# Kernel optimization log

Hardware: AMD Instinct MI355X
Metric: run time of the kernel (lower is better)

## Reference

```python
import jax, jax.numpy as jnp
import numpy as np

K = 3          # attention window (kernel_size)
PAD = 1        # padding
C_IN = 256
C_OUT = 512    # final_channel
N_SPECIES, N_FAMILY, N_ORDER = 64500, 510, 100


def setup_inputs() -> dict:
    key = jax.random.key(0)
    ks = jax.random.split(key, 16)
    B, H, W = 4, 64, 64
    std = 0.01  # per torch.nn.init.normal_(std=0.01)
    inp = {
        "x": jax.random.normal(ks[0], (B, C_IN, H, W), jnp.float32),
        "wq": jax.random.normal(ks[1], (C_OUT, C_IN), jnp.float32) * std,
        "bq": jnp.zeros((C_OUT,), jnp.float32),
        "wk": jax.random.normal(ks[2], (C_OUT, C_IN), jnp.float32) * std,
        "bk": jnp.zeros((C_OUT,), jnp.float32),
        "wv": jax.random.normal(ks[3], (C_OUT, C_IN), jnp.float32) * std,
        "bv": jnp.zeros((C_OUT,), jnp.float32),
        "rel_h": jax.random.normal(ks[4], (C_OUT // 2, K), jnp.float32),
        "rel_w": jax.random.normal(ks[5], (C_OUT // 2, K), jnp.float32),
        "w_species": jax.random.normal(ks[6], (N_SPECIES, C_OUT), jnp.float32) * std,
        "b_species": jnp.zeros((N_SPECIES,), jnp.float32),
        "w_family": jax.random.normal(ks[7], (N_FAMILY, C_OUT), jnp.float32) * std,
        "b_family": jnp.zeros((N_FAMILY,), jnp.float32),
        "w_order": jax.random.normal(ks[8], (N_ORDER, C_OUT), jnp.float32) * std,
        "b_order": jnp.zeros((N_ORDER,), jnp.float32),
    }
    return inp


def _patches(t, H, W):
    # t: padded [B, C, H+2, W+2] -> [B, C, H, W, K, K] (unfold order: kh then kw)
    return jnp.stack([
        jnp.stack([t[:, :, i:i + H, j:j + W] for j in range(K)], axis=-1)
        for i in range(K)], axis=-2)


def _attention_conv(x, wq, bq, wk, bk, wv, bv, rel_h, rel_w):
    B, _, H, W = x.shape
    q = jnp.einsum('oc,bchw->bohw', wq, x) + bq[None, :, None, None]
    k = jnp.einsum('oc,bchw->bohw', wk, x) + bk[None, :, None, None]
    v = jnp.einsum('oc,bchw->bohw', wv, x) + bv[None, :, None, None]
    pad = ((0, 0), (0, 0), (PAD, PAD), (PAD, PAD))
    kp = _patches(jnp.pad(k, pad), H, W)                       # [B,C,H,W,K,K]
    vp = _patches(jnp.pad(v, pad), H, W).reshape(B, C_OUT, H, W, K * K)
    half = C_OUT // 2
    kp = jnp.concatenate([
        kp[:, :half] + rel_h[None, :, None, None, :, None],    # rel over kh
        kp[:, half:] + rel_w[None, :, None, None, None, :],    # rel over kw
    ], axis=1).reshape(B, C_OUT, H, W, K * K)
    attn = jax.nn.softmax(q[..., None] * kp, axis=-1)          # per-channel softmax over window
    return jnp.einsum('bchwk,bchwk->bchw', attn, vp)


def reference(x, wq, bq, wk, bk, wv, bv, rel_h, rel_w,
              w_species, b_species, w_family, b_family, w_order, b_order):
    att = jax.nn.relu(_attention_conv(x, wq, bq, wk, bk, wv, bv, rel_h, rel_w))
    pooled = att.mean(axis=(2, 3))                             # AdaptiveAvgPool2d((1,1)) -> [B, 512]
    sp = pooled @ w_species.T + b_species
    fa = pooled @ w_family.T + b_family
    od = pooled @ w_order.T + b_order
    # concatenated per-level logits (species | family | order)
    return jnp.concatenate([sp, fa, od], axis=1)
```

## Files before the change

### kernel.cpp

```cpp
#include <hip/hip_runtime.h>
#include <stdint.h>

#define HW    4096
#define CIN   256
#define COUT  512
#define NSPE  64500
#define NFAM  510
#define NORD  100
#define NOUT  65110

typedef __attribute__((ext_vector_type(8))) short bf16x8;
typedef __attribute__((ext_vector_type(4))) float f32x4;
typedef __attribute__((address_space(3))) uint32_t lds_u32;
typedef __attribute__((address_space(1))) const uint32_t glob_u32;

__device__ __forceinline__ short f32_to_bf16(float f) {
    uint32_t u = __float_as_uint(f);
    u += 0x7fffu + ((u >> 16) & 1u);
    return (short)(u >> 16);
}
__device__ __forceinline__ float lo16(uint32_t u) {
    return __uint_as_float(u << 16);
}
__device__ __forceinline__ float hi16(uint32_t u) {
    return __uint_as_float(u & 0xffff0000u);
}


__global__ __launch_bounds__(256) void convert_kernel(
    const float* __restrict__ x,
    const float* __restrict__ wq, const float* __restrict__ wk,
    const float* __restrict__ wv,
    short* __restrict__ Xt, short* __restrict__ Wt)
{
    const int t = threadIdx.x;
    __shared__ float lds[32][128];

    if (blockIdx.z < 4) {
        const int kt = blockIdx.x, nt = blockIdx.y, b = blockIdx.z;
        #pragma unroll
        for (int j = 0; j < 16; ++j) {
            int idx = j * 256 + t;
            int c = idx >> 7, p = idx & 127;
            lds[c][p] = x[((size_t)b * CIN + kt * 32 + c) * HW + nt * 128 + p];
        }
        __syncthreads();

        const int n = t >> 1;
        short* out = Xt + (((size_t)(b * 32 + nt) * 8 + kt) << 12);
        union { short s[16]; int4 v[2]; } pk;
        #pragma unroll
        for (int j = 0; j < 16; ++j) {
            int e  = t * 16 + j;
            int sp = (e >> 3) & 3;
            int i  = e & 7;
            int k  = ((sp ^ ((n >> 1) & 3)) << 3) + i;
            pk.s[j] = f32_to_bf16(lds[k][n]);
        }
        int4* dst = (int4*)(out + t * 16);
        dst[0] = pk.v[0];
        dst[1] = pk.v[1];
    } else {
        if (blockIdx.y >= 12) return;
        const int kt = blockIdx.x, mt = blockIdx.y & 3, mat = blockIdx.y >> 2;
        const float* __restrict__ W = (mat == 0) ? wq : (mat == 1) ? wk : wv;
        const int m = t >> 1;
        short* out = Wt + (((size_t)(mat * 4 + mt) * 8 + kt) << 12);

        union { short s[16]; int4 v[2]; } pk;
        #pragma unroll
        for (int j = 0; j < 16; ++j) {
            int e  = t * 16 + j;
            int sp = (e >> 3) & 3;
            int i  = e & 7;
            int k  = ((sp ^ ((m >> 1) & 3)) << 3) + i;
            pk.s[j] = f32_to_bf16(W[(size_t)(mt * 128 + m) * CIN + kt * 32 + k]);
        }
        int4* dst = (int4*)(out + t * 16);
        dst[0] = pk.v[0];
        dst[1] = pk.v[1];
    }
}

__global__ __launch_bounds__(256) void qkv_mfma_kernel(
    const short* __restrict__ Wt, const short* __restrict__ Xt,
    const float* __restrict__ bq, const float* __restrict__ bk,
    const float* __restrict__ bv, short* __restrict__ qkv)
{
    const int nt = blockIdx.x, mt = blockIdx.y, z = blockIdx.z;
    const int mat = z >> 2, b = z & 3;
    const short* At = Wt + (((size_t)(mat * 4 + mt) * 8) << 12);
    const short* Bt = Xt + (((size_t)(b * 32 + nt) * 8) << 12);

    __shared__ __align__(16) short As[2][4096];
    __shared__ __align__(16) short Bs[2][4096];

    const int tid = threadIdx.x, lane = tid & 63, wid = tid >> 6;
    const int wm = wid >> 1, wn = wid & 1;
    const int l15 = lane & 15, sl = lane >> 4;
    const int sw = ((sl ^ ((l15 >> 1) & 3)) << 3);

    f32x4 acc[4][4] = {};

#define STAGE(KT, BUF) do {                                                   \
    _Pragma("unroll")                                                         \
    for (int j = 0; j < 4; ++j) {                                             \
        int li = wid * 4 + j;                                                 \
        if (li < 8)                                                           \
            __builtin_amdgcn_global_load_lds(                                 \
                (glob_u32*)(At + (KT) * 4096 + li * 512 + lane * 8),          \
                (lds_u32*)(&As[BUF][li * 512]), 16, 0, 0);                    \
        else                                                                  \
            __builtin_amdgcn_global_load_lds(                                 \
                (glob_u32*)(Bt + (KT) * 4096 + (li - 8) * 512 + lane * 8),    \
                (lds_u32*)(&Bs[BUF][(li - 8) * 512]), 16, 0, 0);              \
    }                                                                         \
} while (0)

    STAGE(0, 0);
    __syncthreads();

    int buf = 0;
    #pragma unroll 2
    for (int kt = 0; kt < 8; ++kt) {
        if (kt < 7) STAGE(kt + 1, buf ^ 1);

        bf16x8 a[4], bb[4];
        #pragma unroll
        for (int f = 0; f < 4; ++f) {
            int ra = wm * 64 + f * 16 + l15;
            a[f]  = *(const bf16x8*)(&As[buf][ra * 32 + sw]);
            int rb = wn * 64 + f * 16 + l15;
            bb[f] = *(const bf16x8*)(&Bs[buf][rb * 32 + sw]);
        }
        #pragma unroll
        for (int mf = 0; mf < 4; ++mf)
            #pragma unroll
            for (int nf = 0; nf < 4; ++nf)
                acc[mf][nf] = __builtin_amdgcn_mfma_f32_16x16x32_bf16(
                    a[mf], bb[nf], acc[mf][nf], 0, 0, 0);
        __syncthreads();
        buf ^= 1;
    }
#undef STAGE

    const float* bias = (mat == 0) ? bq : (mat == 1) ? bk : bv;
    short* out = qkv + (((size_t)(b * 3 + mat) * COUT + mt * 128) * HW) + nt * 128;
    const int col = lane & 15, g = lane >> 4;
    #pragma unroll
    for (int mf = 0; mf < 4; ++mf) {
        #pragma unroll
        for (int nf = 0; nf < 4; ++nf) {
            #pragma unroll
            for (int r = 0; r < 4; ++r) {
                int m = wm * 64 + mf * 16 + g * 4 + r;
                int n = wn * 64 + nf * 16 + col;
                float val = acc[mf][nf][r] + bias[mt * 128 + m];
                out[(size_t)m * HW + n] = f32_to_bf16(val);
            }
        }
    }
}

__global__ __launch_bounds__(256, 4) void attn_pool_kernel(
    const unsigned short* __restrict__ qkv,
    const float* __restrict__ rel_h, const float* __restrict__ rel_w,
    float* __restrict__ pooled)
{
    const int c = blockIdx.x;
    const int b = blockIdx.y;
    const int tid = threadIdx.x;
    const int h  = tid >> 2;
    const int w0 = (tid & 3) * 16;

    const unsigned short* qc = qkv + ((size_t)(b * 3 + 0) * COUT + c) * HW;
    const unsigned short* kg = qkv + ((size_t)(b * 3 + 1) * COUT + c) * HW;
    const unsigned short* vg = qkv + ((size_t)(b * 3 + 2) * COUT + c) * HW;

    __shared__ float kS[66 * 67];
    __shared__ float vS[66 * 67];
    __shared__ float red[4];

    if (tid < 67) {
        kS[tid] = 0.f;            vS[tid] = 0.f;
        kS[65 * 67 + tid] = 0.f;  vS[65 * 67 + tid] = 0.f;
    }
    if (tid < 64) {
        int r0 = (tid + 1) * 67;
        kS[r0] = 0.f;       vS[r0] = 0.f;
        kS[r0 + 65] = 0.f;  vS[r0 + 65] = 0.f;
    }

    const uint4* kg4 = reinterpret_cast<const uint4*>(kg);
    const uint4* vg4 = reinterpret_cast<const uint4*>(vg);
    #pragma unroll
    for (int it = 0; it < 2; ++it) {
        int ch = tid + it * 256;
        int y = ch >> 3, xs = (ch & 7) * 8;
        uint4 a = kg4[ch];
        float* kp = &kS[(y + 1) * 67 + xs + 1];
        kp[0] = lo16(a.x); kp[1] = hi16(a.x);
        kp[2] = lo16(a.y); kp[3] = hi16(a.y);
        kp[4] = lo16(a.z); kp[5] = hi16(a.z);
        kp[6] = lo16(a.w); kp[7] = hi16(a.w);
        uint4 d = vg4[ch];
        float* vp = &vS[(y + 1) * 67 + xs + 1];
        vp[0] = lo16(d.x); vp[1] = hi16(d.x);
        vp[2] = lo16(d.y); vp[3] = hi16(d.y);
        vp[4] = lo16(d.z); vp[5] = hi16(d.z);
        vp[6] = lo16(d.w); vp[7] = hi16(d.w);
    }

    const float L2E = 1.4426950408889634f;
    float qf[16];
    {
        uint4 qa = *reinterpret_cast<const uint4*>(qc + h * 64 + w0);
        uint4 qb = *reinterpret_cast<const uint4*>(qc + h * 64 + w0 + 8);
        qf[0]  = lo16(qa.x) * L2E; qf[1]  = hi16(qa.x) * L2E;
        qf[2]  = lo16(qa.y) * L2E; qf[3]  = hi16(qa.y) * L2E;
        qf[4]  = lo16(qa.z) * L2E; qf[5]  = hi16(qa.z) * L2E;
        qf[6]  = lo16(qa.w) * L2E; qf[7]  = hi16(qa.w) * L2E;
        qf[8]  = lo16(qb.x) * L2E; qf[9]  = hi16(qb.x) * L2E;
        qf[10] = lo16(qb.y) * L2E; qf[11] = hi16(qb.y) * L2E;
        qf[12] = lo16(qb.z) * L2E; qf[13] = hi16(qb.z) * L2E;
        qf[14] = lo16(qb.w) * L2E; qf[15] = hi16(qb.w) * L2E;
    }

    const bool isH = (c < 256);
    float r3[3];
    #pragma unroll
    for (int i = 0; i < 3; ++i)
        r3[i] = isH ? rel_h[c * 3 + i] : rel_w[(c - 256) * 3 + i];
    float relv[9];
    #pragma unroll
    for (int kh = 0; kh < 3; ++kh)
        #pragma unroll
        for (int kw = 0; kw < 3; ++kw)
            relv[kh * 3 + kw] = isH ? r3[kh] : r3[kw];

    __syncthreads();

    const float* krow = &kS[h * 67 + w0];
    const float* vrow = &vS[h * 67 + w0];

    float kcw[3][3], vcw[3][3];
    #pragma unroll
    for (int s = 0; s < 2; ++s)
        #pragma unroll
        for (int r = 0; r < 3; ++r) {
            kcw[s][r] = krow[r * 67 + s];
            vcw[s][r] = vrow[r * 67 + s];
        }

    float total = 0.f;
    #pragma unroll
    for (int i = 0; i < 16; ++i) {
        const int s2 = (i + 2) % 3;
        #pragma unroll
        for (int r = 0; r < 3; ++r) {
            kcw[s2][r] = krow[r * 67 + i + 2];
            vcw[s2][r] = vrow[r * 67 + i + 2];
        }
        const float q2 = qf[i];
        float num = 0.f, den = 0.f;
        #pragma unroll
        for (int r = 0; r < 3; ++r)
            #pragma unroll
            for (int dx = 0; dx < 3; ++dx) {
                const int sl = (i + dx) % 3;
                float e = __builtin_exp2f(q2 * (kcw[sl][r] + relv[r * 3 + dx]));
                den += e;
                num = fmaf(e, vcw[sl][r], num);
            }
        total += fmaxf(num * __builtin_amdgcn_rcpf(den), 0.f);
    }

    #pragma unroll
    for (int off = 32; off; off >>= 1) total += __shfl_down(total, off);
    if ((tid & 63) == 0) red[tid >> 6] = total;
    __syncthreads();
    if (tid == 0)
        pooled[b * COUT + c] = (red[0] + red[1] + red[2] + red[3]) * (1.f / 4096.f);
}

__global__ __launch_bounds__(256) void heads_kernel(
    const float* __restrict__ pooled,
    const float* __restrict__ w_sp, const float* __restrict__ b_sp,
    const float* __restrict__ w_fa, const float* __restrict__ b_fa,
    const float* __restrict__ w_or, const float* __restrict__ b_or,
    float* __restrict__ out)
{
    const int lane   = threadIdx.x & 63;
    const int wave   = blockIdx.x * (blockDim.x >> 6) + (threadIdx.x >> 6);
    const int nwaves = gridDim.x * (blockDim.x >> 6);

    float pr[4][8];
    #pragma unroll
    for (int b = 0; b < 4; ++b)
        #pragma unroll
        for (int e = 0; e < 8; ++e)
            pr[b][e] = pooled[b * COUT + lane * 8 + e];

    for (int j = wave; j < NOUT; j += nwaves) {
        const float* __restrict__ wrow;
        float bias;
        if (j < NSPE)            { wrow = w_sp + (size_t)j * COUT;          bias = b_sp[j]; }
        else if (j < NSPE + NFAM){ wrow = w_fa + (size_t)(j - NSPE) * COUT; bias = b_fa[j - NSPE]; }
        else                     { wrow = w_or + (size_t)(j - NSPE - NFAM) * COUT; bias = b_or[j - NSPE - NFAM]; }

        const float4 w0 = reinterpret_cast<const float4*>(wrow)[lane * 2 + 0];
        const float4 w1 = reinterpret_cast<const float4*>(wrow)[lane * 2 + 1];
        const float we[8] = {w0.x, w0.y, w0.z, w0.w, w1.x, w1.y, w1.z, w1.w};

        float a0 = 0.f, a1 = 0.f, a2 = 0.f, a3 = 0.f;
        #pragma unroll
        for (int e = 0; e < 8; ++e) {
            a0 += we[e] * pr[0][e];
            a1 += we[e] * pr[1][e];
            a2 += we[e] * pr[2][e];
            a3 += we[e] * pr[3][e];
        }
        #pragma unroll
        for (int off = 32; off; off >>= 1) {
            a0 += __shfl_down(a0, off);
            a1 += __shfl_down(a1, off);
            a2 += __shfl_down(a2, off);
            a3 += __shfl_down(a3, off);
        }
        if (lane == 0) {
            out[0 * NOUT + j] = a0 + bias;
            out[1 * NOUT + j] = a1 + bias;
            out[2 * NOUT + j] = a2 + bias;
            out[3 * NOUT + j] = a3 + bias;
        }
    }
}

extern "C" void kernel_launch(void* const* d_in, const int* in_sizes, int n_in,
                              void* d_out, int out_size, void* d_ws, size_t ws_size,
                              hipStream_t stream) {
    const float* x     = (const float*)d_in[0];
    const float* wq    = (const float*)d_in[1];
    const float* bq    = (const float*)d_in[2];
    const float* wk    = (const float*)d_in[3];
    const float* bk    = (const float*)d_in[4];
    const float* wv    = (const float*)d_in[5];
    const float* bv    = (const float*)d_in[6];
    const float* rel_h = (const float*)d_in[7];
    const float* rel_w = (const float*)d_in[8];
    const float* w_sp  = (const float*)d_in[9];
    const float* b_sp  = (const float*)d_in[10];
    const float* w_fa  = (const float*)d_in[11];
    const float* b_fa  = (const float*)d_in[12];
    const float* w_or  = (const float*)d_in[13];
    const float* b_or  = (const float*)d_in[14];
    float* out = (float*)d_out;

    short* Wt  = (short*)d_ws;
    short* Xt  = Wt + 393216;
    short* qkv = Xt + 4194304;
    float* pooled = (float*)(qkv + 25165824);

    convert_kernel<<<dim3(8, 32, 5), 256, 0, stream>>>(x, wq, wk, wv, Xt, Wt);
    qkv_mfma_kernel<<<dim3(32, 4, 12), 256, 0, stream>>>(Wt, Xt, bq, bk, bv, qkv);
    attn_pool_kernel<<<dim3(COUT, 4), 256, 0, stream>>>(
        (const unsigned short*)qkv, rel_h, rel_w, pooled);
    heads_kernel<<<dim3(2048), 256, 0, stream>>>(
        pooled, w_sp, b_sp, w_fa, b_fa, w_or, b_or, out);
}
```

Baseline: 81.54 us.

## Split attention-pool blocks into two row halves with partial pooled sums

Each attention-pool block now covers 32 image rows plus halo instead of all 64, and the grid doubles along a new z dimension. Each thread handles 8 output pixels instead of 16, and the block's LDS footprint is roughly halved, so occupancy can rise (launch bounds raised to 6). The two half-sums are written to separate pooled buffers and added in the heads kernel. The cost is extra halo row loads, more blocks to launch, and a workspace slot twice as large for pooled.

```diff
diff --git a/kernel.cpp b/kernel.cpp
--- a/kernel.cpp
+++ b/kernel.cpp
@@ -162,68 +162,70 @@
     }
 }
 
-__global__ __launch_bounds__(256, 4) void attn_pool_kernel(
+__global__ __launch_bounds__(256, 6) void attn_pool_kernel(
     const unsigned short* __restrict__ qkv,
     const float* __restrict__ rel_h, const float* __restrict__ rel_w,
-    float* __restrict__ pooled)
+    float* __restrict__ pooledp)
 {
-    const int c = blockIdx.x;
-    const int b = blockIdx.y;
-    const int tid = threadIdx.x;
-    const int h  = tid >> 2;
-    const int w0 = (tid & 3) * 16;
+    const int c    = blockIdx.x;
+    const int b    = blockIdx.y;
+    const int half = blockIdx.z;
+    const int h0   = half * 32;
+    const int tid  = threadIdx.x;
+    const int hr   = tid >> 3;
+    const int w0   = (tid & 7) * 8;
 
     const unsigned short* qc = qkv + ((size_t)(b * 3 + 0) * COUT + c) * HW;
     const unsigned short* kg = qkv + ((size_t)(b * 3 + 1) * COUT + c) * HW;
     const unsigned short* vg = qkv + ((size_t)(b * 3 + 2) * COUT + c) * HW;
 
-    __shared__ float kS[66 * 67];
-    __shared__ float vS[66 * 67];
+    __shared__ float kS[34 * 67];
+    __shared__ float vS[34 * 67];
     __shared__ float red[4];
 
-    if (tid < 67) {
-        kS[tid] = 0.f;            vS[tid] = 0.f;
-        kS[65 * 67 + tid] = 0.f;  vS[65 * 67 + tid] = 0.f;
-    }
-    if (tid < 64) {
-        int r0 = (tid + 1) * 67;
-        kS[r0] = 0.f;       vS[r0] = 0.f;
-        kS[r0 + 65] = 0.f;  vS[r0 + 65] = 0.f;
+    if (tid < 34) {
+        kS[tid * 67] = 0.f;      kS[tid * 67 + 65] = 0.f;
+        vS[tid * 67] = 0.f;      vS[tid * 67 + 65] = 0.f;
     }
 
     const uint4* kg4 = reinterpret_cast<const uint4*>(kg);
     const uint4* vg4 = reinterpret_cast<const uint4*>(vg);
-    #pragma unroll
-    for (int it = 0; it < 2; ++it) {
-        int ch = tid + it * 256;
-        int y = ch >> 3, xs = (ch & 7) * 8;
-        uint4 a = kg4[ch];
-        float* kp = &kS[(y + 1) * 67 + xs + 1];
-        kp[0] = lo16(a.x); kp[1] = hi16(a.x);
-        kp[2] = lo16(a.y); kp[3] = hi16(a.y);
-        kp[4] = lo16(a.z); kp[5] = hi16(a.z);
-        kp[6] = lo16(a.w); kp[7] = hi16(a.w);
-        uint4 d = vg4[ch];
-        float* vp = &vS[(y + 1) * 67 + xs + 1];
-        vp[0] = lo16(d.x); vp[1] = hi16(d.x);
-        vp[2] = lo16(d.y); vp[3] = hi16(d.y);
-        vp[4] = lo16(d.z); vp[5] = hi16(d.z);
-        vp[6] = lo16(d.w); vp[7] = hi16(d.w);
-    }
+
+#define STAGECH(CH) do {                                                      \
+    int lr = (CH) >> 3, cs = ((CH) & 7) * 8;                                  \
+    int gr = h0 - 1 + lr;                                                     \
+    float* kp = &kS[lr * 67 + 1 + cs];                                        \
+    float* vp = &vS[lr * 67 + 1 + cs];                                        \
+    if ((unsigned)gr < 64u) {                                                 \
+        uint4 a = kg4[gr * 8 + ((CH) & 7)];                                   \
+        kp[0] = lo16(a.x); kp[1] = hi16(a.x);                                 \
+        kp[2] = lo16(a.y); kp[3] = hi16(a.y);                                 \
+        kp[4] = lo16(a.z); kp[5] = hi16(a.z);                                 \
+        kp[6] = lo16(a.w); kp[7] = hi16(a.w);                                 \
+        uint4 d = vg4[gr * 8 + ((CH) & 7)];                                   \
+        vp[0] = lo16(d.x); vp[1] = hi16(d.x);                                 \
+        vp[2] = lo16(d.y); vp[3] = hi16(d.y);                                 \
+        vp[4] = lo16(d.z); vp[5] = hi16(d.z);                                 \
+        vp[6] = lo16(d.w); vp[7] = hi16(d.w);                                 \
+    } else {                                                                  \
+        _Pragma("unroll")                                                     \
+        for (int e = 0; e < 8; ++e) { kp[e] = 0.f; vp[e] = 0.f; }             \
+    }                                                                         \
+} while (0)
+
+    STAGECH(tid);
+    if (tid < 16) STAGECH(256 + tid);
+#undef STAGECH
 
     const float L2E = 1.4426950408889634f;
-    float qf[16];
+    const int h = h0 + hr;
+    float qf[8];
     {
         uint4 qa = *reinterpret_cast<const uint4*>(qc + h * 64 + w0);
-        uint4 qb = *reinterpret_cast<const uint4*>(qc + h * 64 + w0 + 8);
-        qf[0]  = lo16(qa.x) * L2E; qf[1]  = hi16(qa.x) * L2E;
-        qf[2]  = lo16(qa.y) * L2E; qf[3]  = hi16(qa.y) * L2E;
-        qf[4]  = lo16(qa.z) * L2E; qf[5]  = hi16(qa.z) * L2E;
-        qf[6]  = lo16(qa.w) * L2E; qf[7]  = hi16(qa.w) * L2E;
-        qf[8]  = lo16(qb.x) * L2E; qf[9]  = hi16(qb.x) * L2E;
-        qf[10] = lo16(qb.y) * L2E; qf[11] = hi16(qb.y) * L2E;
-        qf[12] = lo16(qb.z) * L2E; qf[13] = hi16(qb.z) * L2E;
-        qf[14] = lo16(qb.w) * L2E; qf[15] = hi16(qb.w) * L2E;
+        qf[0] = lo16(qa.x) * L2E; qf[1] = hi16(qa.x) * L2E;
+        qf[2] = lo16(qa.y) * L2E; qf[3] = hi16(qa.y) * L2E;
+        qf[4] = lo16(qa.z) * L2E; qf[5] = hi16(qa.z) * L2E;
+        qf[6] = lo16(qa.w) * L2E; qf[7] = hi16(qa.w) * L2E;
     }
 
     const bool isH = (c < 256);
@@ -240,8 +242,8 @@
 
     __syncthreads();
 
-    const float* krow = &kS[h * 67 + w0];
-    const float* vrow = &vS[h * 67 + w0];
+    const float* krow = &kS[hr * 67 + w0];
+    const float* vrow = &vS[hr * 67 + w0];
 
     float kcw[3][3], vcw[3][3];
     #pragma unroll
@@ -254,7 +256,7 @@
 
     float total = 0.f;
     #pragma unroll
-    for (int i = 0; i < 16; ++i) {
+    for (int i = 0; i < 8; ++i) {
         const int s2 = (i + 2) % 3;
         #pragma unroll
         for (int r = 0; r < 3; ++r) {
@@ -280,11 +282,12 @@
     if ((tid & 63) == 0) red[tid >> 6] = total;
     __syncthreads();
     if (tid == 0)
-        pooled[b * COUT + c] = (red[0] + red[1] + red[2] + red[3]) * (1.f / 4096.f);
+        pooledp[((size_t)half * 4 + b) * COUT + c] =
+            (red[0] + red[1] + red[2] + red[3]) * (1.f / 4096.f);
 }
 
 __global__ __launch_bounds__(256) void heads_kernel(
-    const float* __restrict__ pooled,
+    const float* __restrict__ pooledp,
     const float* __restrict__ w_sp, const float* __restrict__ b_sp,
     const float* __restrict__ w_fa, const float* __restrict__ b_fa,
     const float* __restrict__ w_or, const float* __restrict__ b_or,
@@ -299,7 +302,8 @@
     for (int b = 0; b < 4; ++b)
         #pragma unroll
         for (int e = 0; e < 8; ++e)
-            pr[b][e] = pooled[b * COUT + lane * 8 + e];
+            pr[b][e] = pooledp[(size_t)b * COUT + lane * 8 + e]
+                     + pooledp[(size_t)(4 + b) * COUT + lane * 8 + e];
 
     for (int j = wave; j < NOUT; j += nwaves) {
         const float* __restrict__ wrow;
@@ -359,12 +363,12 @@
     short* Wt  = (short*)d_ws;
     short* Xt  = Wt + 393216;
     short* qkv = Xt + 4194304;
-    float* pooled = (float*)(qkv + 25165824);
+    float* pooledp = (float*)(qkv + 25165824);
 
     convert_kernel<<<dim3(8, 32, 5), 256, 0, stream>>>(x, wq, wk, wv, Xt, Wt);
     qkv_mfma_kernel<<<dim3(32, 4, 12), 256, 0, stream>>>(Wt, Xt, bq, bk, bv, qkv);
-    attn_pool_kernel<<<dim3(COUT, 4), 256, 0, stream>>>(
-        (const unsigned short*)qkv, rel_h, rel_w, pooled);
+    attn_pool_kernel<<<dim3(COUT, 4, 2), 256, 0, stream>>>(
+        (const unsigned short*)qkv, rel_h, rel_w, pooledp);
     heads_kernel<<<dim3(2048), 256, 0, stream>>>(
-        pooled, w_sp, b_sp, w_fa, b_fa, w_or, b_or, out);
-}
+        pooledp, w_sp, b_sp, w_fa, b_fa, w_or, b_or, out);
+}
```

Result: slower. 85.13 us (+4.4%).

## Fuse attention-pool and heads into one launch with cache prefetch and spin-wait

Applied to the files above, without the earlier changes.

Merges the attention/pool kernel and the classifier heads kernel into a single launch. The first 512 blocks touch their rows of head weights early, which is meant to pull them into cache while the attention blocks run, then spin on an atomic counter until all 2048 attention blocks have written pooled results. This hides the head weight streaming (about 133 MB) behind the attention compute and saves one launch. The cost is that the spinning blocks occupy CU slots, and the scheme depends on all attention blocks being able to get scheduled, otherwise it waits until a bounded timeout. It also needs an extra memset per call.

```diff
diff --git a/kernel.cpp b/kernel.cpp
--- a/kernel.cpp
+++ b/kernel.cpp
@@ -8,6 +8,8 @@
 #define NFAM  510
 #define NORD  100
 #define NOUT  65110
+#define NATT  2048
+#define NHB   512
 
 typedef __attribute__((ext_vector_type(8))) short bf16x8;
 typedef __attribute__((ext_vector_type(4))) float f32x4;
@@ -162,24 +164,106 @@
     }
 }
 
-__global__ __launch_bounds__(256, 4) void attn_pool_kernel(
+__global__ __launch_bounds__(256, 4) void attn_heads_kernel(
     const unsigned short* __restrict__ qkv,
     const float* __restrict__ rel_h, const float* __restrict__ rel_w,
-    float* __restrict__ pooled)
+    const float* __restrict__ w_sp, const float* __restrict__ b_sp,
+    const float* __restrict__ w_fa, const float* __restrict__ b_fa,
+    const float* __restrict__ w_or, const float* __restrict__ b_or,
+    float* __restrict__ pooled,
+    int* __restrict__ ctr,
+    float* __restrict__ out)
 {
-    const int c = blockIdx.x;
-    const int b = blockIdx.y;
+    __shared__ float kS[66 * 67];
+    __shared__ float vS[66 * 67];
+    __shared__ float red[4];
+
+    const int bid = blockIdx.x;
     const int tid = threadIdx.x;
+
+    if (bid < NHB) {
+        const int lane = tid & 63, wv = tid >> 6;
+        const int jbase = bid * 128 + wv * 32;
+
+        float ksum = 0.f;
+        for (int r = 0; r < 32; ++r) {
+            int j = jbase + r;
+            if (j < NOUT) {
+                const float* wrow;
+                if (j < NSPE)             wrow = w_sp + (size_t)j * COUT;
+                else if (j < NSPE + NFAM) wrow = w_fa + (size_t)(j - NSPE) * COUT;
+                else                      wrow = w_or + (size_t)(j - NSPE - NFAM) * COUT;
+                float4 a  = reinterpret_cast<const float4*>(wrow)[lane * 2 + 0];
+                float4 b4 = reinterpret_cast<const float4*>(wrow)[lane * 2 + 1];
+                ksum += a.x + a.y + a.z + a.w + b4.x + b4.y + b4.z + b4.w;
+            }
+        }
+        asm volatile("" :: "v"(ksum));
+
+        if (tid == 0) {
+            int it = 0;
+            while (__hip_atomic_load(ctr, __ATOMIC_ACQUIRE,
+                                     __HIP_MEMORY_SCOPE_AGENT) < NATT) {
+                __builtin_amdgcn_s_sleep(4);
+                if (++it > (1 << 22)) break;
+            }
+        }
+        __syncthreads();
+
+        float pr[4][8];
+        #pragma unroll
+        for (int b = 0; b < 4; ++b)
+            #pragma unroll
+            for (int e = 0; e < 8; ++e)
+                pr[b][e] = pooled[b * COUT + lane * 8 + e];
+
+        for (int r = 0; r < 32; ++r) {
+            int j = jbase + r;
+            if (j >= NOUT) break;
+            const float* wrow;
+            float bias;
+            if (j < NSPE)            { wrow = w_sp + (size_t)j * COUT;          bias = b_sp[j]; }
+            else if (j < NSPE + NFAM){ wrow = w_fa + (size_t)(j - NSPE) * COUT; bias = b_fa[j - NSPE]; }
+            else                     { wrow = w_or + (size_t)(j - NSPE - NFAM) * COUT; bias = b_or[j - NSPE - NFAM]; }
+
+            const float4 w0 = reinterpret_cast<const float4*>(wrow)[lane * 2 + 0];
+            const float4 w1 = reinterpret_cast<const float4*>(wrow)[lane * 2 + 1];
+            const float we[8] = {w0.x, w0.y, w0.z, w0.w, w1.x, w1.y, w1.z, w1.w};
+
+            float a0 = 0.f, a1 = 0.f, a2 = 0.f, a3 = 0.f;
+            #pragma unroll
+            for (int e = 0; e < 8; ++e) {
+                a0 += we[e] * pr[0][e];
+                a1 += we[e] * pr[1][e];
+                a2 += we[e] * pr[2][e];
+                a3 += we[e] * pr[3][e];
+            }
+            #pragma unroll
+            for (int off = 32; off; off >>= 1) {
+                a0 += __shfl_down(a0, off);
+                a1 += __shfl_down(a1, off);
+                a2 += __shfl_down(a2, off);
+                a3 += __shfl_down(a3, off);
+            }
+            if (lane == 0) {
+                out[0 * NOUT + j] = a0 + bias;
+                out[1 * NOUT + j] = a1 + bias;
+                out[2 * NOUT + j] = a2 + bias;
+                out[3 * NOUT + j] = a3 + bias;
+            }
+        }
+        return;
+    }
+
+    const int idx = bid - NHB;
+    const int c = idx & 511;
+    const int b = idx >> 9;
     const int h  = tid >> 2;
     const int w0 = (tid & 3) * 16;
 
     const unsigned short* qc = qkv + ((size_t)(b * 3 + 0) * COUT + c) * HW;
     const unsigned short* kg = qkv + ((size_t)(b * 3 + 1) * COUT + c) * HW;
     const unsigned short* vg = qkv + ((size_t)(b * 3 + 2) * COUT + c) * HW;
-
-    __shared__ float kS[66 * 67];
-    __shared__ float vS[66 * 67];
-    __shared__ float red[4];
 
     if (tid < 67) {
         kS[tid] = 0.f;            vS[tid] = 0.f;
@@ -279,60 +363,10 @@
     for (int off = 32; off; off >>= 1) total += __shfl_down(total, off);
     if ((tid & 63) == 0) red[tid >> 6] = total;
     __syncthreads();
-    if (tid == 0)
+    if (tid == 0) {
         pooled[b * COUT + c] = (red[0] + red[1] + red[2] + red[3]) * (1.f / 4096.f);
-}
-
-__global__ __launch_bounds__(256) void heads_kernel(
-    const float* __restrict__ pooled,
-    const float* __restrict__ w_sp, const float* __restrict__ b_sp,
-    const float* __restrict__ w_fa, const float* __restrict__ b_fa,
-    const float* __restrict__ w_or, const float* __restrict__ b_or,
-    float* __restrict__ out)
-{
-    const int lane   = threadIdx.x & 63;
-    const int wave   = blockIdx.x * (blockDim.x >> 6) + (threadIdx.x >> 6);
-    const int nwaves = gridDim.x * (blockDim.x >> 6);
-
-    float pr[4][8];
-    #pragma unroll
-    for (int b = 0; b < 4; ++b)
-        #pragma unroll
-        for (int e = 0; e < 8; ++e)
-            pr[b][e] = pooled[b * COUT + lane * 8 + e];
-
-    for (int j = wave; j < NOUT; j += nwaves) {
-        const float* __restrict__ wrow;
-        float bias;
-        if (j < NSPE)            { wrow = w_sp + (size_t)j * COUT;          bias = b_sp[j]; }
-        else if (j < NSPE + NFAM){ wrow = w_fa + (size_t)(j - NSPE) * COUT; bias = b_fa[j - NSPE]; }
-        else                     { wrow = w_or + (size_t)(j - NSPE - NFAM) * COUT; bias = b_or[j - NSPE - NFAM]; }
-
-        const float4 w0 = reinterpret_cast<const float4*>(wrow)[lane * 2 + 0];
-        const float4 w1 = reinterpret_cast<const float4*>(wrow)[lane * 2 + 1];
-        const float we[8] = {w0.x, w0.y, w0.z, w0.w, w1.x, w1.y, w1.z, w1.w};
-
-        float a0 = 0.f, a1 = 0.f, a2 = 0.f, a3 = 0.f;
-        #pragma unroll
-        for (int e = 0; e < 8; ++e) {
-            a0 += we[e] * pr[0][e];
-            a1 += we[e] * pr[1][e];
-            a2 += we[e] * pr[2][e];
-            a3 += we[e] * pr[3][e];
-        }
-        #pragma unroll
-        for (int off = 32; off; off >>= 1) {
-            a0 += __shfl_down(a0, off);
-            a1 += __shfl_down(a1, off);
-            a2 += __shfl_down(a2, off);
-            a3 += __shfl_down(a3, off);
-        }
-        if (lane == 0) {
-            out[0 * NOUT + j] = a0 + bias;
-            out[1 * NOUT + j] = a1 + bias;
-            out[2 * NOUT + j] = a2 + bias;
-            out[3 * NOUT + j] = a3 + bias;
-        }
+        __threadfence();
+        __hip_atomic_fetch_add(ctr, 1, __ATOMIC_ACQ_REL, __HIP_MEMORY_SCOPE_AGENT);
     }
 }
 
@@ -360,11 +394,12 @@
     short* Xt  = Wt + 393216;
     short* qkv = Xt + 4194304;
     float* pooled = (float*)(qkv + 25165824);
-
+    int*   ctr    = (int*)(pooled + 2048);
+
+    hipMemsetAsync(ctr, 0, sizeof(int), stream);
     convert_kernel<<<dim3(8, 32, 5), 256, 0, stream>>>(x, wq, wk, wv, Xt, Wt);
     qkv_mfma_kernel<<<dim3(32, 4, 12), 256, 0, stream>>>(Wt, Xt, bq, bk, bv, qkv);
-    attn_pool_kernel<<<dim3(COUT, 4), 256, 0, stream>>>(
-        (const unsigned short*)qkv, rel_h, rel_w, pooled);
-    heads_kernel<<<dim3(2048), 256, 0, stream>>>(
-        pooled, w_sp, b_sp, w_fa, b_fa, w_or, b_or, out);
-}
+    attn_heads_kernel<<<dim3(NHB + NATT), 256, 0, stream>>>(
+        (const unsigned short*)qkv, rel_h, rel_w,
+        w_sp, b_sp, w_fa, b_fa, w_or, b_or, pooled, ctr, out);
+}
```

New measurement: 250.0 us. 3.07x slower.

## Prefetch head weights into cache during attention kernel, fold rel-pos bias into FMA

Applied to the files above, without the earlier changes.

Adds 256 extra blocks to the attention-pool launch that stream the species, family and order head weights. The loaded values are summed and discarded, so the weights are warmed into the large last-level cache while attention runs, and the later heads kernel should read them from cache instead of HBM. The attention loop is also split into separate rel_h and rel_w branches that precompute q*rel and use one fmaf inside the exponent. The prefetch blocks compete with the attention blocks for bandwidth and CU slots, and whether the ~132MB of weights stays resident in the MI355X cache is uncertain.

```diff
diff --git a/kernel.cpp b/kernel.cpp
--- a/kernel.cpp
+++ b/kernel.cpp
@@ -8,6 +8,8 @@
 #define NFAM  510
 #define NORD  100
 #define NOUT  65110
+#define NSTR  256
+#define NATT  2048
 
 typedef __attribute__((ext_vector_type(8))) short bf16x8;
 typedef __attribute__((ext_vector_type(4))) float f32x4;
@@ -165,11 +167,36 @@
 __global__ __launch_bounds__(256, 4) void attn_pool_kernel(
     const unsigned short* __restrict__ qkv,
     const float* __restrict__ rel_h, const float* __restrict__ rel_w,
+    const float* __restrict__ w_sp, const float* __restrict__ w_fa,
+    const float* __restrict__ w_or,
     float* __restrict__ pooled)
 {
-    const int c = blockIdx.x;
-    const int b = blockIdx.y;
+    const int bid = blockIdx.x;
     const int tid = threadIdx.x;
+
+    if (bid < NSTR) {
+        const int g = bid * 256 + tid;
+        float s = 0.f;
+        const float4* sp4 = reinterpret_cast<const float4*>(w_sp);
+        for (int idx = g; idx < 8256000; idx += 65536) {
+            float4 t4 = sp4[idx];
+            s += t4.x + t4.y + t4.z + t4.w;
+        }
+        if (g < 65280) {
+            float4 t4 = reinterpret_cast<const float4*>(w_fa)[g];
+            s += t4.x + t4.y + t4.z + t4.w;
+        }
+        if (g < 12800) {
+            float4 t4 = reinterpret_cast<const float4*>(w_or)[g];
+            s += t4.x + t4.y + t4.z + t4.w;
+        }
+        asm volatile("" :: "v"(s));
+        return;
+    }
+
+    const int idx = bid - NSTR;
+    const int c = idx & 511;
+    const int b = idx >> 9;
     const int h  = tid >> 2;
     const int w0 = (tid & 3) * 16;
 
@@ -231,12 +258,6 @@
     #pragma unroll
     for (int i = 0; i < 3; ++i)
         r3[i] = isH ? rel_h[c * 3 + i] : rel_w[(c - 256) * 3 + i];
-    float relv[9];
-    #pragma unroll
-    for (int kh = 0; kh < 3; ++kh)
-        #pragma unroll
-        for (int kw = 0; kw < 3; ++kw)
-            relv[kh * 3 + kw] = isH ? r3[kh] : r3[kw];
 
     __syncthreads();
 
@@ -253,26 +274,52 @@
         }
 
     float total = 0.f;
-    #pragma unroll
-    for (int i = 0; i < 16; ++i) {
-        const int s2 = (i + 2) % 3;
-        #pragma unroll
-        for (int r = 0; r < 3; ++r) {
-            kcw[s2][r] = krow[r * 67 + i + 2];
-            vcw[s2][r] = vrow[r * 67 + i + 2];
-        }
-        const float q2 = qf[i];
-        float num = 0.f, den = 0.f;
-        #pragma unroll
-        for (int r = 0; r < 3; ++r)
-            #pragma unroll
-            for (int dx = 0; dx < 3; ++dx) {
-                const int sl = (i + dx) % 3;
-                float e = __builtin_exp2f(q2 * (kcw[sl][r] + relv[r * 3 + dx]));
-                den += e;
-                num = fmaf(e, vcw[sl][r], num);
+    if (isH) {
+        #pragma unroll
+        for (int i = 0; i < 16; ++i) {
+            const int s2 = (i + 2) % 3;
+            #pragma unroll
+            for (int r = 0; r < 3; ++r) {
+                kcw[s2][r] = krow[r * 67 + i + 2];
+                vcw[s2][r] = vrow[r * 67 + i + 2];
             }
-        total += fmaxf(num * __builtin_amdgcn_rcpf(den), 0.f);
+            const float q2 = qf[i];
+            const float qr[3] = {q2 * r3[0], q2 * r3[1], q2 * r3[2]};
+            float num = 0.f, den = 0.f;
+            #pragma unroll
+            for (int r = 0; r < 3; ++r)
+                #pragma unroll
+                for (int dx = 0; dx < 3; ++dx) {
+                    const int sl = (i + dx) % 3;
+                    float e = __builtin_exp2f(fmaf(q2, kcw[sl][r], qr[r]));
+                    den += e;
+                    num = fmaf(e, vcw[sl][r], num);
+                }
+            total += fmaxf(num * __builtin_amdgcn_rcpf(den), 0.f);
+        }
+    } else {
+        #pragma unroll
+        for (int i = 0; i < 16; ++i) {
+            const int s2 = (i + 2) % 3;
+            #pragma unroll
+            for (int r = 0; r < 3; ++r) {
+                kcw[s2][r] = krow[r * 67 + i + 2];
+                vcw[s2][r] = vrow[r * 67 + i + 2];
+            }
+            const float q2 = qf[i];
+            const float qr[3] = {q2 * r3[0], q2 * r3[1], q2 * r3[2]};
+            float num = 0.f, den = 0.f;
+            #pragma unroll
+            for (int r = 0; r < 3; ++r)
+                #pragma unroll
+                for (int dx = 0; dx < 3; ++dx) {
+                    const int sl = (i + dx) % 3;
+                    float e = __builtin_exp2f(fmaf(q2, kcw[sl][r], qr[dx]));
+                    den += e;
+                    num = fmaf(e, vcw[sl][r], num);
+                }
+            total += fmaxf(num * __builtin_amdgcn_rcpf(den), 0.f);
+        }
     }
 
     #pragma unroll
@@ -363,8 +410,8 @@
 
     convert_kernel<<<dim3(8, 32, 5), 256, 0, stream>>>(x, wq, wk, wv, Xt, Wt);
     qkv_mfma_kernel<<<dim3(32, 4, 12), 256, 0, stream>>>(Wt, Xt, bq, bk, bv, qkv);
-    attn_pool_kernel<<<dim3(COUT, 4), 256, 0, stream>>>(
-        (const unsigned short*)qkv, rel_h, rel_w, pooled);
+    attn_pool_kernel<<<dim3(NSTR + NATT), 256, 0, stream>>>(
+        (const unsigned short*)qkv, rel_h, rel_w, w_sp, w_fa, w_or, pooled);
     heads_kernel<<<dim3(2048), 256, 0, stream>>>(
         pooled, w_sp, b_sp, w_fa, b_fa, w_or, b_or, out);
 }
```

Measured after the change: 95.49 us. +17.1%, slower.
